# Kernel optimization log

Measured on AMD Instinct MI355X. Metric: run time of the kernel, lower is better.

Reference implementation:

```python
import jax, jax.numpy as jnp
import numpy as np

N_CAT = 100000
N_USERS = 50000
D = 64
N_REL = 16  # edge_type in [1, 15]; weight has n_relations-1 = 15 rows
E = 1500000
NNZ = 1500000


def setup_inputs() -> dict:
    key = jax.random.key(0)
    k = jax.random.split(key, 8)
    category_emb = jax.random.normal(k[0], (N_CAT, D), dtype=jnp.float32)
    user_emb = jax.random.normal(k[1], (N_USERS, D), dtype=jnp.float32)
    edge_index = jax.random.randint(k[2], (2, E), 0, N_CAT, dtype=jnp.int32)
    edge_type = jax.random.randint(k[3], (E,), 1, N_REL, dtype=jnp.int32)  # [1, 15]
    iu = jax.random.randint(k[4], (NNZ,), 0, N_USERS, dtype=jnp.int32)
    ic = jax.random.randint(k[5], (NNZ,), 0, N_CAT, dtype=jnp.int32)
    interact_idx = jnp.stack([iu, ic], axis=0)
    interact_val = jax.random.uniform(k[6], (NNZ,), dtype=jnp.float32)
    weight = jax.random.normal(k[7], (N_REL - 1, D), dtype=jnp.float32) * (6.0 / (N_REL - 1 + D)) ** 0.5
    return {"category_emb": category_emb, "user_emb": user_emb,
            "edge_index": edge_index, "edge_type": edge_type,
            "interact_idx": interact_idx, "interact_val": interact_val,
            "weight": weight}


def reference(category_emb, user_emb, edge_index, edge_type, interact_idx, interact_val, weight):
    n_cat = category_emb.shape[0]
    n_users = user_emb.shape[0]
    head, tail = edge_index[0], edge_index[1]

    # per-edge relation embedding gather
    rel = weight[edge_type - 1]                       # [E, d]
    neigh = category_emb[tail] * rel                  # [E, d]

    # norm-based attention score per edge: (||h*r|| * ||t*r||)^2
    hn = jnp.linalg.norm(category_emb[head] * rel, axis=1)   # [E]
    tn = jnp.linalg.norm(neigh, axis=1)                      # [E]
    att = (hn * tn) ** 2                                     # [E]

    # scatter-softmax over head segments (score is constant across feature dim)
    seg_max = jax.ops.segment_max(att, head, num_segments=n_cat)
    e = jnp.exp(att - seg_max[head])
    seg_sum = jax.ops.segment_sum(e, head, num_segments=n_cat)
    w = e / seg_sum[head]                                    # [E]

    # scatter-sum aggregation of weighted neighbor messages
    category_agg = jax.ops.segment_sum(w[:, None] * neigh, head, num_segments=n_cat)  # [n_cat, d]

    # sparse-dense matmul: interact_mat @ category_emb (COO gather + segment_sum)
    iu, ic = interact_idx[0], interact_idx[1]
    user_agg = jax.ops.segment_sum(interact_val[:, None] * category_emb[ic], iu,
                                   num_segments=n_users)     # [n_users, d]

    # relation-score gating of user aggregation
    score = jax.nn.softmax(user_emb @ weight.T, axis=-1)     # [n_users, n_rel-1]
    user_agg = user_agg + (score @ weight) * user_agg
    return category_agg, user_agg
```

## Files before the change

### kernel.cpp

```cpp
#include <hip/hip_runtime.h>

#define N_CAT   100000
#define N_USERS 50000
#define DIM     64
#define N_RELM1 15
#define E_EDGES 1500000
#define NNZ_E   1500000

#define HPB   125
#define NB_H  800
#define UPB   80
#define NB_U  625
#define NB_T  (NB_H + NB_U)
#define CAP8  3072

#define NS_TILES 1563
#define GT_TILES 782
#define HIST_BLKS 256

#define BIN_BLKS 256
#define BIN_CH   5860

#define NTL(p) __builtin_nontemporal_load(p)

__device__ __forceinline__ unsigned short f2bf(float v) {
    unsigned int ub = __float_as_uint(v);
    return (unsigned short)((ub + 0x7FFF + ((ub >> 16) & 1)) >> 16);
}

template <bool USE16>
__global__ void __launch_bounds__(256)
prep_kernel(const float* __restrict__ cat, const float* __restrict__ uemb,
            const float* __restrict__ weight,
            const int* __restrict__ head, const int* __restrict__ iu,
            float* __restrict__ normsq, unsigned short* __restrict__ cat16,
            float* __restrict__ gfac, int* __restrict__ gcnt) {
    __shared__ float smem[8320];
    int t = threadIdx.x;
    int lane = t & 63, wid = t >> 6;
    if (blockIdx.x < NS_TILES) {
        float* c2   = smem;
        float* w2t  = smem + 4160;
        float* nsqT = smem + 5184;
        int nbase = blockIdx.x * 64;
        int nclamp = min(64, N_CAT - nbase);
        for (int i = t; i < 1024; i += 256) {
            int d = i >> 4, r = i & 15;
            float w = (r < N_RELM1) ? weight[r * 64 + d] : 0.f;
            w2t[i] = w * w;
        }
        for (int i = t; i < 4096; i += 256) {
            int row = i >> 6, d = i & 63;
            float v = (row < nclamp) ? cat[(size_t)(nbase + row) * 64 + d] : 0.f;
            c2[row * 65 + d] = v * v;
            if (USE16 && row < nclamp)
                cat16[(size_t)(nbase + row) * 64 + d] = f2bf(v);
        }
        __syncthreads();
        float a0 = 0, a1 = 0, a2 = 0, a3 = 0;
        int r0 = wid * 4;
#pragma unroll 8
        for (int d = 0; d < 64; ++d) {
            float c = c2[lane * 65 + d];
            float4 w4 = *(float4*)&w2t[d * 16 + r0];
            a0 += c * w4.x; a1 += c * w4.y; a2 += c * w4.z; a3 += c * w4.w;
        }
        nsqT[(r0 + 0) * 64 + lane] = a0;
        nsqT[(r0 + 1) * 64 + lane] = a1;
        nsqT[(r0 + 2) * 64 + lane] = a2;
        nsqT[(r0 + 3) * 64 + lane] = a3;
        __syncthreads();
        for (int i = t; i < nclamp * 15; i += 256) {
            int n = i / 15, r = i - n * 15;
            normsq[(size_t)(nbase + n) * 15 + r] = nsqT[r * 64 + n];
        }
    } else if (blockIdx.x < NS_TILES + GT_TILES) {
        float* ut  = smem;
        float* wt  = smem + 4160;
        float* wrT = smem + 5184;
        float* st  = smem + 6208;
        float* pt  = smem + 7232;
        int ub_ = (blockIdx.x - NS_TILES) * 64;
        int uclamp = min(64, N_USERS - ub_);
        for (int i = t; i < 1024; i += 256) {
            int d = i >> 4, r = i & 15;
            float w = (r < N_RELM1) ? weight[r * 64 + d] : 0.f;
            wt[i] = w;
            wrT[r * 64 + d] = w;
        }
        for (int i = t; i < 4096; i += 256) {
            int row = i >> 6, d = i & 63;
            ut[row * 65 + d] = (row < uclamp) ? uemb[(size_t)(ub_ + row) * 64 + d] : 0.f;
        }
        __syncthreads();
        float a0 = 0, a1 = 0, a2 = 0, a3 = 0;
        int r0 = wid * 4;
#pragma unroll 8
        for (int d = 0; d < 64; ++d) {
            float c = ut[lane * 65 + d];
            float4 w4 = *(float4*)&wt[d * 16 + r0];
            a0 += c * w4.x; a1 += c * w4.y; a2 += c * w4.z; a3 += c * w4.w;
        }
        st[lane * 16 + r0 + 0] = a0;
        st[lane * 16 + r0 + 1] = a1;
        st[lane * 16 + r0 + 2] = a2;
        st[lane * 16 + r0 + 3] = a3;
        __syncthreads();
        if (wid == 0) {
            float mx = -1e30f;
            float pv[N_RELM1];
#pragma unroll
            for (int r = 0; r < N_RELM1; ++r) mx = fmaxf(mx, st[lane * 16 + r]);
            float Z = 0.f;
#pragma unroll
            for (int r = 0; r < N_RELM1; ++r) { pv[r] = expf(st[lane * 16 + r] - mx); Z += pv[r]; }
            float inv = 1.f / Z;
#pragma unroll
            for (int r = 0; r < N_RELM1; ++r) pt[lane * 16 + r] = pv[r] * inv;
        }
        __syncthreads();
        for (int i = t; i < uclamp * 64; i += 256) {
            int u = i >> 6, d = i & 63;
            float g = 0.f;
#pragma unroll
            for (int r = 0; r < N_RELM1; ++r) g += pt[u * 16 + r] * wrT[r * 64 + d];
            gfac[(size_t)(ub_ + u) * 64 + d] = g;
        }
    } else {
        int* cnt = (int*)smem;
        for (int i = t; i < NB_T; i += 256) cnt[i] = 0;
        __syncthreads();
        int hb = blockIdx.x - NS_TILES - GT_TILES;
        int stride = HIST_BLKS * 256;
        const unsigned long long* h2 = (const unsigned long long*)head;
        const unsigned long long* u2 = (const unsigned long long*)iu;
        for (int e = hb * 256 + t; e < E_EDGES / 2; e += stride) {
            unsigned long long hv = NTL(&h2[e]);
            atomicAdd(&cnt[((int)hv) / HPB], 1);
            atomicAdd(&cnt[((int)(hv >> 32)) / HPB], 1);
            unsigned long long uv = NTL(&u2[e]);
            atomicAdd(&cnt[NB_H + ((int)uv) / UPB], 1);
            atomicAdd(&cnt[NB_H + ((int)(uv >> 32)) / UPB], 1);
        }
        __syncthreads();
        for (int i = t; i < NB_T; i += 256)
            if (cnt[i]) atomicAdd(&gcnt[i], cnt[i]);
    }
}

__global__ void __launch_bounds__(1024)
bscan_kernel(const int* __restrict__ gcnt,
             int* __restrict__ hbase, int* __restrict__ ubase,
             int* __restrict__ cur) {
    __shared__ int wtot[16];
    int t = threadIdx.x, lane = t & 63, wv = t >> 6;
    int i0 = 2 * t, i1 = 2 * t + 1;
    int c0 = (i0 < NB_T) ? gcnt[i0] : 0;
    int c1 = (i1 < NB_T) ? gcnt[i1] : 0;
    int s = c0 + c1;
    int incl = s;
#pragma unroll
    for (int d = 1; d < 64; d <<= 1) {
        int v = __shfl_up(incl, d, 64);
        if (lane >= d) incl += v;
    }
    if (lane == 63) wtot[wv] = incl;
    __syncthreads();
    int woff = 0;
#pragma unroll
    for (int w = 0; w < 16; ++w) {
        int x = wtot[w];
        if (w < wv) woff += x;
    }
    int excl = woff + incl - s;
    if (i0 < NB_T) {
        if (i0 < NB_H) { hbase[i0] = excl; cur[i0] = excl; }
        else { int v = excl - E_EDGES; ubase[i0 - NB_H] = v; cur[i0] = v; }
    }
    int e1 = excl + c0;
    if (i1 < NB_T) {
        if (i1 < NB_H) { hbase[i1] = e1; cur[i1] = e1; }
        else { int v = e1 - E_EDGES; ubase[i1 - NB_H] = v; cur[i1] = v; }
    }
    if (t == 0) { hbase[NB_H] = E_EDGES; ubase[NB_U] = NNZ_E; }
}

__device__ __forceinline__ void scan_reserve(int* __restrict__ cnt, int* __restrict__ lofs,
                                             int* __restrict__ gbase, int* __restrict__ cur,
                                             int* __restrict__ wtot) {
    int t = threadIdx.x, lane = t & 63, wv = t >> 6;
    int i0 = 2 * t, i1 = 2 * t + 1;
    int a0 = (i0 < NB_T) ? cnt[i0] : 0;
    int a1 = (i1 < NB_T) ? cnt[i1] : 0;
    int s = a0 + a1, incl = s;
#pragma unroll
    for (int d = 1; d < 64; d <<= 1) {
        int v = __shfl_up(incl, d, 64);
        if (lane >= d) incl += v;
    }
    if (lane == 63) wtot[wv] = incl;
    __syncthreads();
    int woff = 0;
#pragma unroll
    for (int w = 0; w < 16; ++w) { int x = wtot[w]; if (w < wv) woff += x; }
    int excl = woff + incl - s;
    if (i0 < NB_T) lofs[i0] = excl;
    if (i1 < NB_T) lofs[i1] = excl + a0;
    for (int i = t; i < NB_T; i += 1024) {
        int c = cnt[i];
        gbase[i] = c ? atomicAdd(&cur[i], c) : 0;
    }
    __syncthreads();
}

__global__ void __launch_bounds__(1024)
binning_kernel(const int* __restrict__ head, const int* __restrict__ tail,
               const int* __restrict__ etype,
               const int* __restrict__ iu, const int* __restrict__ ic,
               const float* __restrict__ ival,
               int* __restrict__ cur,
               int* __restrict__ ebinned, unsigned long long* __restrict__ nbinned) {
    __shared__ int cnt[NB_T];
    __shared__ int lofs[NB_T];
    __shared__ int gbase[NB_T];
    __shared__ int wtot[16];
    __shared__ int stage[BIN_CH];
    __shared__ unsigned short sbk[BIN_CH];
    int t = threadIdx.x;
    int c0 = blockIdx.x * BIN_CH;
    int c1 = min(c0 + BIN_CH, E_EDGES);

    for (int i = t; i < NB_T; i += 1024) cnt[i] = 0;
    __syncthreads();
    for (int e = c0 + t; e < c1; e += 1024)
        atomicAdd(&cnt[NTL(&head[e]) / HPB], 1);
    __syncthreads();
    scan_reserve(cnt, lofs, gbase, cur, wtot);
    for (int i = t; i < NB_T; i += 1024) cnt[i] = 0;
    __syncthreads();
    for (int e = c0 + t; e < c1; e += 1024) {
        int h = NTL(&head[e]);
        int b = h / HPB;
        int r = atomicAdd(&cnt[b], 1);
        int slot = lofs[b] + r;
        stage[slot] = ((h - b * HPB) << 21) | (NTL(&tail[e]) << 4) | (NTL(&etype[e]) - 1);
        sbk[slot] = (unsigned short)b;
    }
    __syncthreads();
    int cn = c1 - c0;
    for (int s = t; s < cn; s += 1024) {
        int bk = sbk[s];
        ebinned[gbase[bk] + (s - lofs[bk])] = stage[s];
    }
    __syncthreads();

    int2* stage2 = (int2*)stage;
    int2* nb2 = (int2*)nbinned;
#pragma unroll 1
    for (int half = 0; half < 2; ++half) {
        int h0 = c0 + half * (BIN_CH / 2);
        int h1 = min(h0 + BIN_CH / 2, E_EDGES);
        for (int i = t; i < NB_T; i += 1024) cnt[i] = 0;
        __syncthreads();
        for (int e = h0 + t; e < h1; e += 1024)
            atomicAdd(&cnt[NB_H + NTL(&iu[e]) / UPB], 1);
        __syncthreads();
        scan_reserve(cnt, lofs, gbase, cur, wtot);
        for (int i = t; i < NB_T; i += 1024) cnt[i] = 0;
        __syncthreads();
        for (int e = h0 + t; e < h1; e += 1024) {
            int u = NTL(&iu[e]);
            int b = NB_H + u / UPB;
            int r = atomicAdd(&cnt[b], 1);
            int slot = lofs[b] + r;
            stage2[slot] = make_int2(((u - (b - NB_H) * UPB) << 17) | NTL(&ic[e]),
                                     __float_as_int(NTL(&ival[e])));
            sbk[slot] = (unsigned short)b;
        }
        __syncthreads();
        int hn = h1 - h0;
        for (int s = t; s < hn; s += 1024) {
            int bk = sbk[s];
            nb2[gbase[bk] + (s - lofs[bk])] = stage2[s];
        }
        __syncthreads();
    }
}

template <bool USE16>
__global__ void __launch_bounds__(512)
fused_agg(const int* __restrict__ ebinned, const int* __restrict__ hbase,
          const unsigned long long* __restrict__ nbinned, const int* __restrict__ ubase,
          const float* __restrict__ normsq, const float* __restrict__ catf,
          const unsigned short* __restrict__ cat16,
          const float* __restrict__ weight,
          float* __restrict__ catagg, float* __restrict__ useragg) {
    __shared__ unsigned long long buf8[CAP8];
    __shared__ float4 wlds4[N_RELM1 * 16];
    __shared__ float hn[HPB * N_RELM1];
    __shared__ int cnt[HPB];
    __shared__ int ofs[HPB + 1];
    __shared__ unsigned int mxu[HPB];
    __shared__ float Zs[HPB];
    const uint2*  c16r = (const uint2*)cat16;
    const float4* cfr  = (const float4*)catf;
    int t = threadIdx.x;
    int wid = t >> 6, lane = t & 63;
    int qlane = lane & 15, qid = lane >> 4;

    if (blockIdx.x < NB_H) {
        int b = blockIdx.x;
        int s0 = hbase[b];
        int n = min(hbase[b + 1] - s0, CAP8);
        for (int i = t; i < N_RELM1 * 16; i += 512)
            wlds4[i] = ((const float4*)weight)[i];
        for (int i = t; i < HPB * N_RELM1; i += 512)
            hn[i] = normsq[(size_t)b * HPB * N_RELM1 + i];
        for (int i = t; i < HPB; i += 512) { cnt[i] = 0; mxu[i] = 0u; Zs[i] = 0.f; }
        __syncthreads();
        for (int i = t; i < n; i += 512)
            atomicAdd(&cnt[ebinned[s0 + i] >> 21], 1);
        __syncthreads();
        if (wid == 0) {
            int i0 = 2 * lane, i1 = 2 * lane + 1;
            int c0 = (i0 < HPB) ? cnt[i0] : 0;
            int c1 = (i1 < HPB) ? cnt[i1] : 0;
            int s = c0 + c1, incl = s;
#pragma unroll
            for (int d = 1; d < 64; d <<= 1) {
                int v = __shfl_up(incl, d, 64);
                if (lane >= d) incl += v;
            }
            int excl = incl - s;
            if (i0 <= HPB) ofs[i0] = excl;
            if (i1 <= HPB) ofs[i1] = excl + c0;
        }
        __syncthreads();
        for (int i = t; i < HPB; i += 512) cnt[i] = 0;
        __syncthreads();
        for (int i = t; i < n; i += 512) {
            int pk = ebinned[s0 + i];
            int hl = pk >> 21, tj = (pk >> 4) & 0x1FFFF, rj = pk & 15;
            float att = hn[hl * N_RELM1 + rj] * normsq[(size_t)tj * N_RELM1 + rj];
            int r = atomicAdd(&cnt[hl], 1);
            buf8[ofs[hl] + r] = ((unsigned long long)__float_as_uint(att) << 32) | (unsigned int)pk;
            atomicMax(&mxu[hl], __float_as_uint(att));
        }
        __syncthreads();
        for (int i = t; i < n; i += 512) {
            unsigned long long pay = buf8[i];
            int hl = ((int)(unsigned int)pay) >> 21;
            float att = __uint_as_float((unsigned int)(pay >> 32));
            float w = expf(att - __uint_as_float(mxu[hl]));
            ((unsigned int*)buf8)[2 * i + 1] = __float_as_uint(w);
            atomicAdd(&Zs[hl], w);
        }
        __syncthreads();
        for (int hl = wid; hl < HPB; hl += 8) {
            int h = b * HPB + hl;
            int e0 = ofs[hl], e1 = ofs[hl + 1];
            float invZ = (e1 > e0) ? 1.f / Zs[hl] : 0.f;
            float ax = 0.f, ay = 0.f, az = 0.f, aw = 0.f;
            for (int j = e0; j < e1; j += 16) {
#pragma unroll
                for (int k = 0; k < 4; ++k) {
                    int idx = j + k * 4 + qid;
                    bool ok = idx < e1;
                    idx = ok ? idx : e0;
                    unsigned long long pay = buf8[idx];
                    int pk = (int)(unsigned int)pay;
                    float w = ok ? __uint_as_float((unsigned int)(pay >> 32)) : 0.f;
                    int tj = (pk >> 4) & 0x1FFFF, rj = pk & 15;
                    float c0, c1, c2, c3;
                    if (USE16) {
                        uint2 uv = c16r[(size_t)tj * 16 + qlane];
                        c0 = __uint_as_float(uv.x << 16);
                        c1 = __uint_as_float(uv.x & 0xFFFF0000u);
                        c2 = __uint_as_float(uv.y << 16);
                        c3 = __uint_as_float(uv.y & 0xFFFF0000u);
                    } else {
                        float4 cv = cfr[(size_t)tj * 16 + qlane];
                        c0 = cv.x; c1 = cv.y; c2 = cv.z; c3 = cv.w;
                    }
                    float4 wl = wlds4[rj * 16 + qlane];
                    ax += w * c0 * wl.x;
                    ay += w * c1 * wl.y;
                    az += w * c2 * wl.z;
                    aw += w * c3 * wl.w;
                }
            }
            ax += __shfl_xor(ax, 16, 64); ax += __shfl_xor(ax, 32, 64);
            ay += __shfl_xor(ay, 16, 64); ay += __shfl_xor(ay, 32, 64);
            az += __shfl_xor(az, 16, 64); az += __shfl_xor(az, 32, 64);
            aw += __shfl_xor(aw, 16, 64); aw += __shfl_xor(aw, 32, 64);
            if (lane < 16)
                ((float4*)catagg)[(size_t)h * 16 + qlane] =
                    make_float4(ax * invZ, ay * invZ, az * invZ, aw * invZ);
        }
    } else {
        int ub = blockIdx.x - NB_H;
        int s0 = ubase[ub];
        int n = min(ubase[ub + 1] - s0, CAP8);
        for (int i = t; i < UPB; i += 512) cnt[i] = 0;
        __syncthreads();
        for (int i = t; i < n; i += 512)
            atomicAdd(&cnt[((unsigned int)nbinned[s0 + i]) >> 17], 1);
        __syncthreads();
        if (wid == 0) {
            int i0 = 2 * lane, i1 = 2 * lane + 1;
            int c0 = (i0 < UPB) ? cnt[i0] : 0;
            int c1 = (i1 < UPB) ? cnt[i1] : 0;
            int s = c0 + c1, incl = s;
#pragma unroll
            for (int d = 1; d < 64; d <<= 1) {
                int v = __shfl_up(incl, d, 64);
                if (lane >= d) incl += v;
            }
            int excl = incl - s;
            if (i0 <= UPB) ofs[i0] = excl;
            if (i1 <= UPB) ofs[i1] = excl + c0;
        }
        __syncthreads();
        for (int i = t; i < UPB; i += 512) cnt[i] = 0;
        __syncthreads();
        for (int i = t; i < n; i += 512) {
            unsigned long long pay = nbinned[s0 + i];
            int ul = ((unsigned int)pay) >> 17;
            int r = atomicAdd(&cnt[ul], 1);
            buf8[ofs[ul] + r] = pay;
        }
        __syncthreads();
        for (int ul = wid; ul < UPB; ul += 8) {
            int u = ub * UPB + ul;
            int e0 = ofs[ul], e1 = ofs[ul + 1];
            float ax = 0.f, ay = 0.f, az = 0.f, aw = 0.f;
            for (int j = e0; j < e1; j += 32) {
#pragma unroll
                for (int k = 0; k < 8; ++k) {
                    int idx = j + k * 4 + qid;
                    bool ok = idx < e1;
                    idx = ok ? idx : e0;
                    unsigned long long pay = buf8[idx];
                    float v = ok ? __uint_as_float((unsigned int)(pay >> 32)) : 0.f;
                    int c = (int)((unsigned int)pay & 0x1FFFFu);
                    float c0, c1, c2, c3;
                    if (USE16) {
                        uint2 uv = c16r[(size_t)c * 16 + qlane];
                        c0 = __uint_as_float(uv.x << 16);
                        c1 = __uint_as_float(uv.x & 0xFFFF0000u);
                        c2 = __uint_as_float(uv.y << 16);
                        c3 = __uint_as_float(uv.y & 0xFFFF0000u);
                    } else {
                        float4 cv = cfr[(size_t)c * 16 + qlane];
                        c0 = cv.x; c1 = cv.y; c2 = cv.z; c3 = cv.w;
                    }
                    ax += v * c0;
                    ay += v * c1;
                    az += v * c2;
                    aw += v * c3;
                }
            }
            ax += __shfl_xor(ax, 16, 64); ax += __shfl_xor(ax, 32, 64);
            ay += __shfl_xor(ay, 16, 64); ay += __shfl_xor(ay, 32, 64);
            az += __shfl_xor(az, 16, 64); az += __shfl_xor(az, 32, 64);
            aw += __shfl_xor(aw, 16, 64); aw += __shfl_xor(aw, 32, 64);
            if (lane < 16) {
                float4 gf = ((float4*)useragg)[(size_t)u * 16 + qlane];
                ((float4*)useragg)[(size_t)u * 16 + qlane] =
                    make_float4(ax * (1.f + gf.x), ay * (1.f + gf.y),
                                az * (1.f + gf.z), aw * (1.f + gf.w));
            }
        }
    }
}

extern "C" void kernel_launch(void* const* d_in, const int* in_sizes, int n_in,
                              void* d_out, int out_size, void* d_ws, size_t ws_size,
                              hipStream_t stream) {
    const float* cat    = (const float*)d_in[0];
    const float* uemb   = (const float*)d_in[1];
    const int*   eidx   = (const int*)d_in[2];
    const int*   etype  = (const int*)d_in[3];
    const int*   iidx   = (const int*)d_in[4];
    const float* ival   = (const float*)d_in[5];
    const float* weight = (const float*)d_in[6];

    float* catagg  = (float*)d_out;
    float* useragg = (float*)d_out + (size_t)N_CAT * DIM;

    int* ws = (int*)d_ws;
    float* normsq   = (float*)ws;
    int*   ebinned  = ws + 1500000;
    unsigned long long* nbinned = (unsigned long long*)(ws + 3000000);
    int*   gcnt     = ws + 6000000;
    int*   hbase    = ws + 6001425;
    int*   ubase    = ws + 6002226;
    int*   cur      = ws + 6002852;
    unsigned short* cat16 = (unsigned short*)(ws + 6004278);
    const size_t NEED16 = (size_t)(6004278 + 3200000) * 4;
    bool use16 = ws_size >= NEED16;

    const int* head = eidx;
    const int* tail = eidx + E_EDGES;
    const int* iu   = iidx;
    const int* ic   = iidx + NNZ_E;

    hipMemsetAsync(gcnt, 0, (size_t)NB_T * sizeof(int), stream);

    if (use16) {
        prep_kernel<true><<<NS_TILES + GT_TILES + HIST_BLKS, 256, 0, stream>>>(
            cat, uemb, weight, head, iu, normsq, cat16, useragg, gcnt);
    } else {
        prep_kernel<false><<<NS_TILES + GT_TILES + HIST_BLKS, 256, 0, stream>>>(
            cat, uemb, weight, head, iu, normsq, cat16, useragg, gcnt);
    }
    bscan_kernel<<<1, 1024, 0, stream>>>(gcnt, hbase, ubase, cur);
    binning_kernel<<<BIN_BLKS, 1024, 0, stream>>>(head, tail, etype, iu, ic, ival,
                                                  cur, ebinned, nbinned);
    if (use16) {
        fused_agg<true><<<NB_T, 512, 0, stream>>>(
            ebinned, hbase, nbinned, ubase, normsq, cat, cat16, weight, catagg, useragg);
    } else {
        fused_agg<false><<<NB_T, 512, 0, stream>>>(
            ebinned, hbase, nbinned, ubase, normsq, cat, cat16, weight, catagg, useragg);
    }
}
```

Before: 203.9 us.

## Reuse per-chunk histograms from prep kernel in binning pass, widen gather unroll

```diff
diff --git a/kernel.cpp b/kernel.cpp
--- a/kernel.cpp
+++ b/kernel.cpp
@@ -16,7 +16,6 @@
 
 #define NS_TILES 1563
 #define GT_TILES 782
-#define HIST_BLKS 256
 
 #define BIN_BLKS 256
 #define BIN_CH   5860
@@ -34,7 +33,9 @@
             const float* __restrict__ weight,
             const int* __restrict__ head, const int* __restrict__ iu,
             float* __restrict__ normsq, unsigned short* __restrict__ cat16,
-            float* __restrict__ gfac, int* __restrict__ gcnt) {
+            float* __restrict__ gfac, int* __restrict__ gcnt,
+            int* __restrict__ cnts_cat, int* __restrict__ cnts_u0,
+            int* __restrict__ cnts_u1) {
     __shared__ float smem[8320];
     int t = threadIdx.x;
     int lane = t & 63, wid = t >> 6;
@@ -127,24 +128,32 @@
             gfac[(size_t)(ub_ + u) * 64 + d] = g;
         }
     } else {
-        int* cnt = (int*)smem;
-        for (int i = t; i < NB_T; i += 256) cnt[i] = 0;
+        int* ccnt = (int*)smem;
+        int* cu0  = ccnt + NB_H;
+        int* cu1  = cu0 + 640;
+        for (int i = t; i < NB_H + 1280; i += 256) ccnt[i] = 0;
         __syncthreads();
         int hb = blockIdx.x - NS_TILES - GT_TILES;
-        int stride = HIST_BLKS * 256;
-        const unsigned long long* h2 = (const unsigned long long*)head;
-        const unsigned long long* u2 = (const unsigned long long*)iu;
-        for (int e = hb * 256 + t; e < E_EDGES / 2; e += stride) {
-            unsigned long long hv = NTL(&h2[e]);
-            atomicAdd(&cnt[((int)hv) / HPB], 1);
-            atomicAdd(&cnt[((int)(hv >> 32)) / HPB], 1);
-            unsigned long long uv = NTL(&u2[e]);
-            atomicAdd(&cnt[NB_H + ((int)uv) / UPB], 1);
-            atomicAdd(&cnt[NB_H + ((int)(uv >> 32)) / UPB], 1);
-        }
-        __syncthreads();
-        for (int i = t; i < NB_T; i += 256)
-            if (cnt[i]) atomicAdd(&gcnt[i], cnt[i]);
+        int c0 = hb * BIN_CH;
+        int c1 = min(c0 + BIN_CH, E_EDGES);
+        int hmid = c0 + BIN_CH / 2;
+        for (int e = c0 + t; e < c1; e += 256) {
+            atomicAdd(&ccnt[NTL(&head[e]) / HPB], 1);
+            int ub = NTL(&iu[e]) / UPB;
+            atomicAdd((e < hmid) ? &cu0[ub] : &cu1[ub], 1);
+        }
+        __syncthreads();
+        for (int i = t; i < NB_H; i += 256) {
+            int v = ccnt[i];
+            cnts_cat[hb * NB_H + i] = v;
+            if (v) atomicAdd(&gcnt[i], v);
+        }
+        for (int j = t; j < NB_U; j += 256) {
+            int v0 = cu0[j], v1 = cu1[j];
+            cnts_u0[hb * 640 + j] = v0;
+            cnts_u1[hb * 640 + j] = v1;
+            if (v0 + v1) atomicAdd(&gcnt[NB_H + j], v0 + v1);
+        }
     }
 }
 
@@ -185,13 +194,14 @@
     if (t == 0) { hbase[NB_H] = E_EDGES; ubase[NB_U] = NNZ_E; }
 }
 
-__device__ __forceinline__ void scan_reserve(int* __restrict__ cnt, int* __restrict__ lofs,
-                                             int* __restrict__ gbase, int* __restrict__ cur,
-                                             int* __restrict__ wtot) {
+__device__ __forceinline__ void block_scan_excl(const int* __restrict__ cnt,
+                                                int* __restrict__ lofs, int n,
+                                                int* __restrict__ wtot) {
+    __syncthreads();
     int t = threadIdx.x, lane = t & 63, wv = t >> 6;
-    int i0 = 2 * t, i1 = 2 * t + 1;
-    int a0 = (i0 < NB_T) ? cnt[i0] : 0;
-    int a1 = (i1 < NB_T) ? cnt[i1] : 0;
+    int i0 = 2 * t, i1 = i0 + 1;
+    int a0 = (i0 < n) ? cnt[i0] : 0;
+    int a1 = (i1 < n) ? cnt[i1] : 0;
     int s = a0 + a1, incl = s;
 #pragma unroll
     for (int d = 1; d < 64; d <<= 1) {
@@ -204,12 +214,8 @@
 #pragma unroll
     for (int w = 0; w < 16; ++w) { int x = wtot[w]; if (w < wv) woff += x; }
     int excl = woff + incl - s;
-    if (i0 < NB_T) lofs[i0] = excl;
-    if (i1 < NB_T) lofs[i1] = excl + a0;
-    for (int i = t; i < NB_T; i += 1024) {
-        int c = cnt[i];
-        gbase[i] = c ? atomicAdd(&cur[i], c) : 0;
-    }
+    if (i0 < n) lofs[i0] = excl;
+    if (i1 < n) lofs[i1] = excl + a0;
     __syncthreads();
 }
 
@@ -218,30 +224,34 @@
                const int* __restrict__ etype,
                const int* __restrict__ iu, const int* __restrict__ ic,
                const float* __restrict__ ival,
+               const int* __restrict__ cnts_cat, const int* __restrict__ cnts_u0,
+               const int* __restrict__ cnts_u1,
                int* __restrict__ cur,
                int* __restrict__ ebinned, unsigned long long* __restrict__ nbinned) {
-    __shared__ int cnt[NB_T];
-    __shared__ int lofs[NB_T];
-    __shared__ int gbase[NB_T];
+    __shared__ int scnt[NB_H];
+    __shared__ int lofs[NB_H];
+    __shared__ int gbase[NB_H];
     __shared__ int wtot[16];
     __shared__ int stage[BIN_CH];
     __shared__ unsigned short sbk[BIN_CH];
     int t = threadIdx.x;
-    int c0 = blockIdx.x * BIN_CH;
+    int hb = blockIdx.x;
+    int c0 = hb * BIN_CH;
     int c1 = min(c0 + BIN_CH, E_EDGES);
 
-    for (int i = t; i < NB_T; i += 1024) cnt[i] = 0;
-    __syncthreads();
-    for (int e = c0 + t; e < c1; e += 1024)
-        atomicAdd(&cnt[NTL(&head[e]) / HPB], 1);
-    __syncthreads();
-    scan_reserve(cnt, lofs, gbase, cur, wtot);
-    for (int i = t; i < NB_T; i += 1024) cnt[i] = 0;
+    for (int i = t; i < NB_H; i += 1024) scnt[i] = NTL(&cnts_cat[hb * NB_H + i]);
+    block_scan_excl(scnt, lofs, NB_H, wtot);
+    for (int i = t; i < NB_H; i += 1024) {
+        int c = scnt[i];
+        gbase[i] = c ? atomicAdd(&cur[i], c) : 0;
+    }
+    __syncthreads();
+    for (int i = t; i < NB_H; i += 1024) scnt[i] = 0;
     __syncthreads();
     for (int e = c0 + t; e < c1; e += 1024) {
         int h = NTL(&head[e]);
         int b = h / HPB;
-        int r = atomicAdd(&cnt[b], 1);
+        int r = atomicAdd(&scnt[b], 1);
         int slot = lofs[b] + r;
         stage[slot] = ((h - b * HPB) << 21) | (NTL(&tail[e]) << 4) | (NTL(&etype[e]) - 1);
         sbk[slot] = (unsigned short)b;
@@ -252,7 +262,6 @@
         int bk = sbk[s];
         ebinned[gbase[bk] + (s - lofs[bk])] = stage[s];
     }
-    __syncthreads();
 
     int2* stage2 = (int2*)stage;
     int2* nb2 = (int2*)nbinned;
@@ -260,20 +269,23 @@
     for (int half = 0; half < 2; ++half) {
         int h0 = c0 + half * (BIN_CH / 2);
         int h1 = min(h0 + BIN_CH / 2, E_EDGES);
-        for (int i = t; i < NB_T; i += 1024) cnt[i] = 0;
-        __syncthreads();
-        for (int e = h0 + t; e < h1; e += 1024)
-            atomicAdd(&cnt[NB_H + NTL(&iu[e]) / UPB], 1);
-        __syncthreads();
-        scan_reserve(cnt, lofs, gbase, cur, wtot);
-        for (int i = t; i < NB_T; i += 1024) cnt[i] = 0;
+        const int* crow = half ? cnts_u1 : cnts_u0;
+        __syncthreads();
+        for (int i = t; i < NB_U; i += 1024) scnt[i] = NTL(&crow[hb * 640 + i]);
+        block_scan_excl(scnt, lofs, NB_U, wtot);
+        for (int i = t; i < NB_U; i += 1024) {
+            int c = scnt[i];
+            gbase[i] = c ? atomicAdd(&cur[NB_H + i], c) : 0;
+        }
+        __syncthreads();
+        for (int i = t; i < NB_U; i += 1024) scnt[i] = 0;
         __syncthreads();
         for (int e = h0 + t; e < h1; e += 1024) {
             int u = NTL(&iu[e]);
-            int b = NB_H + u / UPB;
-            int r = atomicAdd(&cnt[b], 1);
+            int b = u / UPB;
+            int r = atomicAdd(&scnt[b], 1);
             int slot = lofs[b] + r;
-            stage2[slot] = make_int2(((u - (b - NB_H) * UPB) << 17) | NTL(&ic[e]),
+            stage2[slot] = make_int2(((u - b * UPB) << 17) | NTL(&ic[e]),
                                      __float_as_int(NTL(&ival[e])));
             sbk[slot] = (unsigned short)b;
         }
@@ -283,7 +295,6 @@
             int bk = sbk[s];
             nb2[gbase[bk] + (s - lofs[bk])] = stage2[s];
         }
-        __syncthreads();
     }
 }
 
@@ -361,9 +372,9 @@
             int e0 = ofs[hl], e1 = ofs[hl + 1];
             float invZ = (e1 > e0) ? 1.f / Zs[hl] : 0.f;
             float ax = 0.f, ay = 0.f, az = 0.f, aw = 0.f;
-            for (int j = e0; j < e1; j += 16) {
-#pragma unroll
-                for (int k = 0; k < 4; ++k) {
+            for (int j = e0; j < e1; j += 32) {
+#pragma unroll
+                for (int k = 0; k < 8; ++k) {
                     int idx = j + k * 4 + qid;
                     bool ok = idx < e1;
                     idx = ok ? idx : e0;
@@ -500,6 +511,11 @@
     const size_t NEED16 = (size_t)(6004278 + 3200000) * 4;
     bool use16 = ws_size >= NEED16;
 
+    int* dscr     = (int*)d_out;
+    int* cnts_cat = dscr;
+    int* cnts_u0  = dscr + 256 * NB_H;
+    int* cnts_u1  = cnts_u0 + 256 * 640;
+
     const int* head = eidx;
     const int* tail = eidx + E_EDGES;
     const int* iu   = iidx;
@@ -508,14 +524,17 @@
     hipMemsetAsync(gcnt, 0, (size_t)NB_T * sizeof(int), stream);
 
     if (use16) {
-        prep_kernel<true><<<NS_TILES + GT_TILES + HIST_BLKS, 256, 0, stream>>>(
-            cat, uemb, weight, head, iu, normsq, cat16, useragg, gcnt);
+        prep_kernel<true><<<NS_TILES + GT_TILES + BIN_BLKS, 256, 0, stream>>>(
+            cat, uemb, weight, head, iu, normsq, cat16, useragg, gcnt,
+            cnts_cat, cnts_u0, cnts_u1);
     } else {
-        prep_kernel<false><<<NS_TILES + GT_TILES + HIST_BLKS, 256, 0, stream>>>(
-            cat, uemb, weight, head, iu, normsq, cat16, useragg, gcnt);
+        prep_kernel<false><<<NS_TILES + GT_TILES + BIN_BLKS, 256, 0, stream>>>(
+            cat, uemb, weight, head, iu, normsq, cat16, useragg, gcnt,
+            cnts_cat, cnts_u0, cnts_u1);
     }
     bscan_kernel<<<1, 1024, 0, stream>>>(gcnt, hbase, ubase, cur);
     binning_kernel<<<BIN_BLKS, 1024, 0, stream>>>(head, tail, etype, iu, ic, ival,
+                                                  cnts_cat, cnts_u0, cnts_u1,
                                                   cur, ebinned, nbinned);
     if (use16) {
         fused_agg<true><<<NB_T, 512, 0, stream>>>(
```

Result: slower. 212.3 us (+4.1%).
